# Kernel optimization log

Hardware: AMD Instinct MI355X
Metric: run time of the kernel (lower is better)

Reference implementation:

```python
import jax, jax.numpy as jnp
import numpy as np

DIM = 1024
HEADS = 16
HEAD_DIM = DIM // HEADS


def setup_inputs() -> dict:
    key = jax.random.key(0)
    ks = jax.random.split(key, 9)
    s = 1.0 / np.sqrt(DIM)
    return {
        "x": jax.random.normal(ks[0], (2, 2048, 1, DIM), dtype=jnp.float32),
        "Wq": jax.random.normal(ks[1], (DIM, DIM), dtype=jnp.float32) * s,
        "bq": jnp.zeros((DIM,), dtype=jnp.float32),
        "Wk": jax.random.normal(ks[2], (DIM, DIM), dtype=jnp.float32) * s,
        "bk": jnp.zeros((DIM,), dtype=jnp.float32),
        "Wv": jax.random.normal(ks[3], (DIM, DIM), dtype=jnp.float32) * s,
        "bv": jnp.zeros((DIM,), dtype=jnp.float32),
        "Wo": jax.random.normal(ks[4], (DIM, DIM), dtype=jnp.float32) * s,
        "bo": jnp.zeros((DIM,), dtype=jnp.float32),
    }


def reference(x, Wq, bq, Wk, bk, Wv, bv, Wo, bo):
    b, t, _, d = x.shape
    h, hd = HEADS, HEAD_DIM
    # torch Linear: y = x @ W.T + b
    q = (x @ Wq.T + bq).reshape(b, t, h, hd)
    k = (x @ Wk.T + bk).reshape(b, t, h, hd)
    v = (x @ Wv.T + bv).reshape(b, t, h, hd)
    # Source applies self.scaling (hd**-0.5) in torch AND divides by
    # sqrt(k_features) inside the jax chunk routine -> net scale 1/hd.
    q = q * (1.0 / hd)
    # key_chunk_size >= T -> one chunk; online softmax == exact stable softmax
    scores = jnp.einsum('bqhd,bkhd->bhqk', q, k)  # [B,H,T,T]
    w = jax.nn.softmax(scores, axis=-1)
    o = jnp.einsum('bhqk,bkhd->bqhd', w, v).reshape(b, t, d)
    return o @ Wo.T + bo
```

## Files before the change

kernel.cpp:

```cpp
#include <hip/hip_runtime.h>
#include <math.h>

typedef _Float16 f16;
typedef _Float16 f16x2 __attribute__((ext_vector_type(2)));
typedef _Float16 f16x4 __attribute__((ext_vector_type(4)));
typedef _Float16 f16x8 __attribute__((ext_vector_type(8)));
typedef float    f32x4 __attribute__((ext_vector_type(4)));

constexpr int DIM   = 1024;
constexpr int HEADS = 16;
constexpr int HD    = 64;
constexpr int BATCH = 2;
constexpr int SEQ   = 2048;
constexpr int MTOT  = BATCH * SEQ;
constexpr int NT2   = SEQ / 128;

#define QSCALE (1.4426950408889634f / 64.0f)

#define MFMA16(a, b, c) __builtin_amdgcn_mfma_f32_16x16x32_f16((a), (b), (c), 0, 0, 0)

__device__ __forceinline__ void glds16(const void* g, void* l) {
    __builtin_amdgcn_global_load_lds(
        (const __attribute__((address_space(1))) void*)g,
        (__attribute__((address_space(3))) void*)l, 16, 0, 0);
}

__device__ __forceinline__ float exp2_hw(float x) {
    float r;
    asm("v_exp_f32 %0, %1" : "=v"(r) : "v"(x));
    return r;
}

__device__ __forceinline__ f16x2 pk_f16(float a, float b) {
    return __builtin_bit_cast(f16x2, __builtin_amdgcn_cvt_pkrtz(a, b));
}

__global__ __launch_bounds__(256) void presplit_kernel(
    const float* __restrict__ x,  const float* __restrict__ Wq,
    const float* __restrict__ Wk, const float* __restrict__ Wv,
    const float* __restrict__ Wo,
    f16* __restrict__ Xh,  f16* __restrict__ WqH, f16* __restrict__ WkH,
    f16* __restrict__ WvH, f16* __restrict__ WoH)
{
    const int bid = blockIdx.x;
    const float* src; f16* dh; int row;
    if (bid < 4096)      { src = x;  dh = Xh;  row = bid; }
    else if (bid < 5120) { src = Wq; dh = WqH; row = bid - 4096; }
    else if (bid < 6144) { src = Wk; dh = WkH; row = bid - 5120; }
    else if (bid < 7168) { src = Wv; dh = WvH; row = bid - 6144; }
    else                 { src = Wo; dh = WoH; row = bid - 7168; }

    const int k = threadIdx.x * 4;
    const float4 v = *reinterpret_cast<const float4*>(&src[(size_t)row * DIM + k]);
    const int s = (row >> 1) & 3;
    const size_t o = (size_t)row * DIM + (k & ~31) + ((k & 31) ^ (s << 3));
    f16x4 h4;
    h4[0] = (f16)v.x; h4[1] = (f16)v.y; h4[2] = (f16)v.z; h4[3] = (f16)v.w;
    *reinterpret_cast<f16x4*>(&dh[o]) = h4;
}

template <int MODE>
__device__ __forceinline__ void gemm_plane_body(
    const f16* __restrict__ AhG, const f16* __restrict__ BhG,
    const float* __restrict__ bias, float* __restrict__ C,
    f16* __restrict__ F, float scale, f16* __restrict__ smem)
{
    const int tid = threadIdx.x;
    const int l   = tid & 63;
    const int w   = tid >> 6;
    const int wm  = (w >> 1) * 64;
    const int wn  = (w & 1) * 64;
    const int m0  = blockIdx.y * 128;
    const int n0  = blockIdx.x * 128;
    const int fr  = l & 15;
    const int fk  = (l >> 4) * 8;
    const int rg  = (l >> 4) * 4;
    const int fko = fk ^ (((fr >> 1) & 3) << 3);

    f32x4 acc[4][4] = {};

#define GSTAGE(B, K0) do {                                                  \
        _Pragma("unroll")                                                   \
        for (int j = 0; j < 4; ++j) {                                       \
            const int c = w * 4 + j;                             \
            const int p = c >> 3;                         \
            const f16* P = (p == 0) ? AhG : BhG;                            \
            const int r0 = (p == 0) ? m0 : n0;                              \
            const int row = r0 + (c & 7) * 16 + (l >> 2);                   \
            glds16(P + (size_t)row * DIM + (K0) + (l & 3) * 8,              \
                   smem + (B) * 8192 + c * 512);                            \
        }                                                                   \
    } while (0)

    GSTAGE(0, 0);
    GSTAGE(1, 32);
    int b0 = 0, b1 = 1, b2 = 2;

    for (int k0 = 0; k0 < DIM; k0 += 32) {
        if (k0 + 64 < DIM) {
            GSTAGE(b2, k0 + 64);
            asm volatile("s_waitcnt vmcnt(8)\ns_barrier" ::: "memory");
        } else if (k0 + 32 < DIM) {
            asm volatile("s_waitcnt vmcnt(4)\ns_barrier" ::: "memory");
        } else {
            asm volatile("s_waitcnt vmcnt(0)\ns_barrier" ::: "memory");
        }

        const f16* Ah = smem + b0 * 8192;
        const f16* Bh = Ah + 4096;

        f16x8 ah[4], bh[4];
        #pragma unroll
        for (int m = 0; m < 4; ++m)
            ah[m] = *reinterpret_cast<const f16x8*>(&Ah[(wm + m * 16 + fr) * 32 + fko]);
        #pragma unroll
        for (int n = 0; n < 4; ++n)
            bh[n] = *reinterpret_cast<const f16x8*>(&Bh[(wn + n * 16 + fr) * 32 + fko]);
        #pragma unroll
        for (int n = 0; n < 4; ++n)
            #pragma unroll
            for (int m = 0; m < 4; ++m) {
                if (MODE == 1)
                    acc[m][n] = MFMA16(bh[n], ah[m], acc[m][n]);
                else
                    acc[m][n] = MFMA16(ah[m], bh[n], acc[m][n]);
            }
        asm volatile("s_barrier" ::: "memory");
        const int tmp = b0; b0 = b1; b1 = b2; b2 = tmp;
    }
#undef GSTAGE

    if (MODE == 0 || MODE == 3) {
        #pragma unroll
        for (int n = 0; n < 4; ++n) {
            const int col  = n0 + wn + n * 16 + fr;
            const float bb = bias[col];
            #pragma unroll
            for (int m = 0; m < 4; ++m) {
                #pragma unroll
                for (int r = 0; r < 4; ++r) {
                    const int row = m0 + wm + m * 16 + rg + r;
                    const float v = (acc[m][n][r] + bb) * scale;
                    if (MODE == 0) C[(size_t)row * DIM + col] = v;
                    else           F[(size_t)row * DIM + col] = (f16)v;
                }
            }
        }
    } else if (MODE == 1) {
        constexpr int RS = 72;
        const int batch = m0 >> 11;
        const int kvg0  = m0 & 2047;
        for (int s = 0; s < 2; ++s) {
            __syncthreads();
            if ((w & 1) == s) {
                #pragma unroll
                for (int n = 0; n < 4; ++n) {
                    #pragma unroll
                    for (int m = 0; m < 4; ++m) {
                        const int kvrow = wm + m * 16 + fr;
                        const int dd    = n * 16 + rg;
                        f16x4 h4;
                        #pragma unroll
                        for (int r = 0; r < 4; ++r)
                            h4[r] = (f16)(acc[m][n][r] + bias[n0 + wn + dd + r]);
                        const int o = kvrow * RS + (dd ^ ((kvrow & 7) << 3));
                        *reinterpret_cast<f16x4*>(&smem[o]) = h4;
                    }
                }
            }
            __syncthreads();
            const size_t bh_ = (size_t)batch * HEADS + (n0 >> 6) + s;
            const int row = tid >> 1, c0 = (tid & 1) * 32;
            #pragma unroll
            for (int j = 0; j < 4; ++j) {
                const int so = row * RS + c0 + j * 8;
                const size_t go = bh_ * 131072 + (size_t)(kvg0 + row) * 64 + c0 + j * 8;
                *reinterpret_cast<f16x8*>(&F[go]) =
                    *reinterpret_cast<const f16x8*>(&smem[so]);
            }
        }
    } else {
        constexpr int RS = 136;
        const int batch = m0 >> 11;
        const int kvg0  = m0 & 2047;
        for (int s = 0; s < 2; ++s) {
            __syncthreads();
            if ((w & 1) == s) {
                #pragma unroll
                for (int n = 0; n < 4; ++n) {
                    const int d    = n * 16 + fr;
                    const float bb = bias[n0 + wn + d];
                    #pragma unroll
                    for (int m = 0; m < 4; ++m) {
                        const int kvl = wm + m * 16 + rg;
                        f16x4 h4;
                        h4[0] = (f16)(acc[m][n][0] + bb);
                        h4[1] = (f16)(acc[m][n][1] + bb);
                        h4[2] = (f16)(acc[m][n][2] + bb);
                        h4[3] = (f16)(acc[m][n][3] + bb);
                        const int o = d * RS + (kvl ^ ((d & 7) << 3));
                        *reinterpret_cast<f16x4*>(&smem[o]) = h4;
                    }
                }
            }
            __syncthreads();
            const size_t bh_ = (size_t)batch * HEADS + (n0 >> 6) + s;
            const int row = tid >> 2, c0 = (tid & 3) * 32;
            #pragma unroll
            for (int j = 0; j < 4; ++j) {
                const int so = row * RS + c0 + j * 8;
                const size_t go = bh_ * 131072 + (size_t)row * 2048 + kvg0 + c0 + j * 8;
                *reinterpret_cast<f16x8*>(&F[go]) =
                    *reinterpret_cast<const f16x8*>(&smem[so]);
            }
        }
    }
}

__global__ __launch_bounds__(256) void qkv_kernel(
    const f16* __restrict__ XhG,
    const f16* __restrict__ WqH, const float* __restrict__ bq,
    const f16* __restrict__ WkH, const float* __restrict__ bk,
    const f16* __restrict__ WvH, const float* __restrict__ bv,
    f16* __restrict__ QhG, f16* __restrict__ KhG, f16* __restrict__ VhG)
{
    __shared__ __align__(16) f16 smem[24576];
    if (blockIdx.z == 0)
        gemm_plane_body<3>(XhG, WqH, bq, nullptr, QhG, QSCALE, smem);
    else if (blockIdx.z == 1)
        gemm_plane_body<1>(XhG, WkH, bk, nullptr, KhG, 1.0f, smem);
    else
        gemm_plane_body<2>(XhG, WvH, bv, nullptr, VhG, 1.0f, smem);
}

__global__ __launch_bounds__(256) void oproj_kernel(
    const f16* __restrict__ OhG, const f16* __restrict__ WoH,
    const float* __restrict__ bo, float* __restrict__ out)
{
    __shared__ __align__(16) f16 smem[24576];
    gemm_plane_body<0>(OhG, WoH, bo, out, nullptr, 1.0f, smem);
}

__global__ __launch_bounds__(256, 2) void attn_kernel(
    const f16* __restrict__ QhG, const f16* __restrict__ KhG,
    const f16* __restrict__ VhG, f16* __restrict__ OhG)
{
    __shared__ __align__(16) f16 lds[2][2][8192];
    __shared__ __align__(16) f16 PL[4][2][1024];

    const int tid = threadIdx.x;
    const int l   = tid & 63;
    const int w   = tid >> 6;
    const int fr  = l & 15;
    const int g   = l >> 4;
    const int fk  = g * 8;
    const int rg  = g * 4;
    const int swz = (fr & 7) << 3;

    const int lin  = blockIdx.x + 16 * (blockIdx.y + 16 * blockIdx.z);
    const int sid  = (lin & 7) * 64 + (lin >> 3);
    const int qblk = sid & 15;
    const int head = (sid >> 4) & 15;
    const int batch = sid >> 8;

    const int q0 = qblk * 128;
    const size_t rowbase = (size_t)batch * SEQ;
    const int hcol = head * HD;
    const size_t bhbase = ((size_t)batch * HEADS + head) * (size_t)(SEQ * HD);

    size_t kA[4], vA[4];
    #pragma unroll
    for (int c = 0; c < 4; ++c) {
        const int h0 = (w * 4 + c) * 512 + l * 8;
        kA[c] = bhbase + (size_t)h0;
        vA[c] = bhbase + (size_t)(h0 >> 7) * 2048 + (h0 & 127);
    }

#define STAGE(B, T) do {                                                    \
        const size_t _ko = (size_t)(T) * 8192;                              \
        const size_t _vo = (size_t)(T) * 128;                               \
        _Pragma("unroll")                                                   \
        for (int c = 0; c < 4; ++c) {                                       \
            const int lo_ = (w * 4 + c) * 512;                              \
            glds16(KhG + kA[c] + _ko, &lds[B][0][lo_]);                     \
            glds16(VhG + vA[c] + _vo, &lds[B][1][lo_]);                     \
        }                                                                   \
    } while (0)

    STAGE(0, 0);

    f16x8 qh[2][2];
    #pragma unroll
    for (int qb = 0; qb < 2; ++qb) {
        const f16* qp = &QhG[(rowbase + q0 + w * 32 + qb * 16 + fr) * DIM + hcol];
        qh[qb][0] = *reinterpret_cast<const f16x8*>(&qp[fk]);
        qh[qb][1] = *reinterpret_cast<const f16x8*>(&qp[32 + fk]);
    }

    f16x8 onesv;
    #pragma unroll
    for (int i = 0; i < 8; ++i) onesv[i] = (f16)1.0f;

    f32x4 ls[2] = {};
    f32x4 oa[4][2] = {};

    int cur = 0;
    for (int t = 0; t < NT2; ++t) {
        asm volatile("s_waitcnt vmcnt(0) lgkmcnt(0)\ns_barrier" ::: "memory");
        if (t + 1 < NT2) STAGE(cur ^ 1, t + 1);

        #pragma unroll
        for (int hh = 0; hh < 2; ++hh) {
            const f16* Kh = &lds[cur][0][hh * 4096];
            const f16* Vh = &lds[cur][1][hh * 64];

            f32x4 sa[4][2] = {};
            __builtin_amdgcn_s_setprio(1);
            #pragma unroll
            for (int kvb = 0; kvb < 4; ++kvb) {
                #pragma unroll
                for (int ks = 0; ks < 2; ++ks) {
                    const int o = ((kvb * 16 + fr) * 64 + ks * 32 + fk) ^ swz;
                    const f16x8 kh = *reinterpret_cast<const f16x8*>(&Kh[o]);
                    sa[kvb][0] = MFMA16(kh, qh[0][ks], sa[kvb][0]);
                    sa[kvb][1] = MFMA16(kh, qh[1][ks], sa[kvb][1]);
                }
            }
            __builtin_amdgcn_s_setprio(0);

            f16x8 pf[2][2];
            #pragma unroll
            for (int qb = 0; qb < 2; ++qb) {
                f16* Wh = &PL[w][qb][0];
                #pragma unroll
                for (int kvb = 0; kvb < 4; ++kvb) {
                    const f16x2 p01 = pk_f16(exp2_hw(sa[kvb][qb][0]),
                                             exp2_hw(sa[kvb][qb][1]));
                    const f16x2 p23 = pk_f16(exp2_hw(sa[kvb][qb][2]),
                                             exp2_hw(sa[kvb][qb][3]));
                    f16x4 h4;
                    h4[0] = p01[0]; h4[1] = p01[1]; h4[2] = p23[0]; h4[3] = p23[1];
                    const int po = (fr * 64 + kvb * 16 + rg) ^ swz;
                    *reinterpret_cast<f16x4*>(&Wh[po]) = h4;
                }
                #pragma unroll
                for (int ks = 0; ks < 2; ++ks) {
                    const int ro = (fr * 64 + ks * 32 + fk) ^ swz;
                    pf[qb][ks] = *reinterpret_cast<const f16x8*>(&Wh[ro]);
                }
            }

            __builtin_amdgcn_s_setprio(1);
            #pragma unroll
            for (int qb = 0; qb < 2; ++qb)
                #pragma unroll
                for (int ks = 0; ks < 2; ++ks)
                    ls[qb] = MFMA16(onesv, pf[qb][ks], ls[qb]);
            #pragma unroll
            for (int db = 0; db < 4; ++db) {
                #pragma unroll
                for (int ks = 0; ks < 2; ++ks) {
                    const int vo = (db * 16 + fr) * 128 + ((ks * 32 + fk) ^ swz);
                    const f16x8 vh = *reinterpret_cast<const f16x8*>(&Vh[vo]);
                    oa[db][0] = MFMA16(vh, pf[0][ks], oa[db][0]);
                    oa[db][1] = MFMA16(vh, pf[1][ks], oa[db][1]);
                }
            }
            __builtin_amdgcn_s_setprio(0);
        }
        cur ^= 1;
    }
#undef STAGE

    #pragma unroll
    for (int qb = 0; qb < 2; ++qb) {
        const float inv = 1.0f / ls[qb][0];
        const size_t row = rowbase + q0 + w * 32 + qb * 16 + fr;
        const int s = ((int)row >> 1) & 3;
        #pragma unroll
        for (int db = 0; db < 4; ++db) {
            f16x4 h4;
            #pragma unroll
            for (int j = 0; j < 4; ++j) h4[j] = (f16)(oa[db][qb][j] * inv);
            const int kg = hcol + db * 16 + rg;
            const size_t o = row * DIM + (kg & ~31) + ((kg & 31) ^ (s << 3));
            *reinterpret_cast<f16x4*>(&OhG[o]) = h4;
        }
    }
}

extern "C" void kernel_launch(void* const* d_in, const int* in_sizes, int n_in,
                              void* d_out, int out_size, void* d_ws, size_t ws_size,
                              hipStream_t stream)
{
    const float* x  = (const float*)d_in[0];
    const float* Wq = (const float*)d_in[1];
    const float* bq = (const float*)d_in[2];
    const float* Wk = (const float*)d_in[3];
    const float* bk = (const float*)d_in[4];
    const float* Wv = (const float*)d_in[5];
    const float* bv = (const float*)d_in[6];
    const float* Wo = (const float*)d_in[7];
    const float* bo = (const float*)d_in[8];
    float* out = (float*)d_out;

    const size_t PS = (size_t)MTOT * DIM;
    f16* QhG = (f16*)d_ws;
    f16* KhG = QhG + PS;
    f16* VhG = KhG + PS;
    f16* XhG = VhG + PS;
    f16* WqH = XhG + PS;
    f16* WkH = WqH + (size_t)DIM * DIM;
    f16* WvH = WkH + (size_t)DIM * DIM;
    f16* WoH = WvH + (size_t)DIM * DIM;
    f16* OhG = XhG;

    presplit_kernel<<<8192, 256, 0, stream>>>(x, Wq, Wk, Wv, Wo,
                                              XhG, WqH, WkH, WvH, WoH);

    dim3 gqkv(DIM / 128, MTOT / 128, 3);
    qkv_kernel<<<gqkv, 256, 0, stream>>>(XhG, WqH, bq, WkH, bk, WvH, bv,
                                         QhG, KhG, VhG);

    dim3 gattn(SEQ / 128, HEADS, BATCH);
    attn_kernel<<<gattn, 256, 0, stream>>>(QhG, KhG, VhG, OhG);

    dim3 gout(DIM / 128, MTOT / 128);
    oproj_kernel<<<gout, 256, 0, stream>>>(OhG, WoH, bo, out);
}
```

Before: 112.4 us.

## Fuse Q, K, V projections into one block sharing the X tile

The QKV projection now runs one block per output tile that computes Q, K and V together. Each of the four waves stages one operand (X, Wq, Wk or Wv), so the X tile is loaded from global memory once instead of three times. The block keeps three accumulator sets and uses 96KB of shared memory with launch bounds of one block per CU. That cuts the grid to a third and lowers occupancy, and with fewer blocks per CU the load latency may be harder to hide. The attention kernel's V staging addresses and LDS offsets are also rewritten to a 64-wide row stride.

Result: no change. 110.9 us (-1.4%).

```diff
diff --git a/kernel.cpp b/kernel.cpp
--- a/kernel.cpp
+++ b/kernel.cpp
@@ -59,12 +59,15 @@
     *reinterpret_cast<f16x4*>(&dh[o]) = h4;
 }
 
-template <int MODE>
-__device__ __forceinline__ void gemm_plane_body(
-    const f16* __restrict__ AhG, const f16* __restrict__ BhG,
-    const float* __restrict__ bias, float* __restrict__ C,
-    f16* __restrict__ F, float scale, f16* __restrict__ smem)
-{
+__global__ __launch_bounds__(256, 1) void qkv_kernel(
+    const f16* __restrict__ XhG,
+    const f16* __restrict__ WqH, const float* __restrict__ bq,
+    const f16* __restrict__ WkH, const float* __restrict__ bk,
+    const f16* __restrict__ WvH, const float* __restrict__ bv,
+    f16* __restrict__ QhG, f16* __restrict__ KhG, f16* __restrict__ VhG)
+{
+    __shared__ __align__(16) f16 smem[49152];
+
     const int tid = threadIdx.x;
     const int l   = tid & 63;
     const int w   = tid >> 6;
@@ -77,13 +80,168 @@
     const int rg  = (l >> 4) * 4;
     const int fko = fk ^ (((fr >> 1) & 3) << 3);
 
+    const f16* Pw = (w == 0) ? XhG : (w == 1) ? WqH : (w == 2) ? WkH : WvH;
+    const int  r0w = (w == 0) ? m0 : n0;
+
+    f32x4 accq[4][4] = {}, acck[4][4] = {}, accv[4][4] = {};
+
+#define GSTAGE(B, K0) do {                                                  \
+        _Pragma("unroll")                                                   \
+        for (int j = 0; j < 8; ++j) {                                       \
+            const int row = r0w + j * 16 + (l >> 2);                        \
+            glds16(Pw + (size_t)row * DIM + (K0) + (l & 3) * 8,             \
+                   smem + (B) * 16384 + w * 4096 + j * 512);                \
+        }                                                                   \
+    } while (0)
+
+    GSTAGE(0, 0);
+    GSTAGE(1, 32);
+    int b0 = 0, b1 = 1, b2 = 2;
+
+    for (int k0 = 0; k0 < DIM; k0 += 32) {
+        if (k0 + 64 < DIM) {
+            GSTAGE(b2, k0 + 64);
+            asm volatile("s_waitcnt vmcnt(16)\ns_barrier" ::: "memory");
+        } else if (k0 + 32 < DIM) {
+            asm volatile("s_waitcnt vmcnt(8)\ns_barrier" ::: "memory");
+        } else {
+            asm volatile("s_waitcnt vmcnt(0)\ns_barrier" ::: "memory");
+        }
+
+        const f16* Bu = smem + b0 * 16384;
+        f16x8 ah[4], bqf[4], bkf[4], bvf[4];
+        #pragma unroll
+        for (int m = 0; m < 4; ++m)
+            ah[m] = *reinterpret_cast<const f16x8*>(&Bu[(wm + m * 16 + fr) * 32 + fko]);
+        #pragma unroll
+        for (int n = 0; n < 4; ++n) {
+            const int r = (wn + n * 16 + fr) * 32 + fko;
+            bqf[n] = *reinterpret_cast<const f16x8*>(&Bu[4096 + r]);
+            bkf[n] = *reinterpret_cast<const f16x8*>(&Bu[8192 + r]);
+            bvf[n] = *reinterpret_cast<const f16x8*>(&Bu[12288 + r]);
+        }
+        #pragma unroll
+        for (int n = 0; n < 4; ++n)
+            #pragma unroll
+            for (int m = 0; m < 4; ++m) {
+                accq[m][n] = MFMA16(ah[m], bqf[n], accq[m][n]);
+                acck[m][n] = MFMA16(bkf[n], ah[m], acck[m][n]);
+                accv[m][n] = MFMA16(ah[m], bvf[n], accv[m][n]);
+            }
+        asm volatile("s_barrier" ::: "memory");
+        const int tmp = b0; b0 = b1; b1 = b2; b2 = tmp;
+    }
+#undef GSTAGE
+
+    #pragma unroll
+    for (int n = 0; n < 4; ++n) {
+        const int col  = n0 + wn + n * 16 + fr;
+        const float bb = bq[col];
+        #pragma unroll
+        for (int m = 0; m < 4; ++m)
+            #pragma unroll
+            for (int r = 0; r < 4; ++r) {
+                const int row = m0 + wm + m * 16 + rg + r;
+                QhG[(size_t)row * DIM + col] = (f16)((accq[m][n][r] + bb) * QSCALE);
+            }
+    }
+
+    const int batch = m0 >> 11;
+    const int kvg0  = m0 & 2047;
+
+    {
+        constexpr int RS = 72;
+        for (int s = 0; s < 2; ++s) {
+            __syncthreads();
+            if ((w & 1) == s) {
+                #pragma unroll
+                for (int n = 0; n < 4; ++n) {
+                    #pragma unroll
+                    for (int m = 0; m < 4; ++m) {
+                        const int kvrow = wm + m * 16 + fr;
+                        const int dd    = n * 16 + rg;
+                        f16x4 h4;
+                        #pragma unroll
+                        for (int r = 0; r < 4; ++r)
+                            h4[r] = (f16)(acck[m][n][r] + bk[n0 + wn + dd + r]);
+                        const int o = kvrow * RS + (dd ^ ((kvrow & 7) << 3));
+                        *reinterpret_cast<f16x4*>(&smem[o]) = h4;
+                    }
+                }
+            }
+            __syncthreads();
+            const size_t bh_ = (size_t)batch * HEADS + (n0 >> 6) + s;
+            const int row = tid >> 1, c0 = (tid & 1) * 32;
+            #pragma unroll
+            for (int j = 0; j < 4; ++j) {
+                const int so = row * RS + c0 + j * 8;
+                const size_t go = bh_ * 131072 + (size_t)(kvg0 + row) * 64 + c0 + j * 8;
+                *reinterpret_cast<f16x8*>(&KhG[go]) =
+                    *reinterpret_cast<const f16x8*>(&smem[so]);
+            }
+        }
+    }
+
+    {
+        constexpr int RS = 136;
+        for (int s = 0; s < 2; ++s) {
+            __syncthreads();
+            if ((w & 1) == s) {
+                #pragma unroll
+                for (int n = 0; n < 4; ++n) {
+                    const int d    = n * 16 + fr;
+                    const float bb = bv[n0 + wn + d];
+                    #pragma unroll
+                    for (int m = 0; m < 4; ++m) {
+                        const int kvl = wm + m * 16 + rg;
+                        f16x4 h4;
+                        h4[0] = (f16)(accv[m][n][0] + bb);
+                        h4[1] = (f16)(accv[m][n][1] + bb);
+                        h4[2] = (f16)(accv[m][n][2] + bb);
+                        h4[3] = (f16)(accv[m][n][3] + bb);
+                        const int o = d * RS + (kvl ^ ((d & 7) << 3));
+                        *reinterpret_cast<f16x4*>(&smem[o]) = h4;
+                    }
+                }
+            }
+            __syncthreads();
+            const size_t bh_ = (size_t)batch * HEADS + (n0 >> 6) + s;
+            const int row = tid >> 2, c0 = (tid & 3) * 32;
+            #pragma unroll
+            for (int j = 0; j < 4; ++j) {
+                const int so = row * RS + c0 + j * 8;
+                const size_t go = bh_ * 131072 + (size_t)row * 2048 + kvg0 + c0 + j * 8;
+                *reinterpret_cast<f16x8*>(&VhG[go]) =
+                    *reinterpret_cast<const f16x8*>(&smem[so]);
+            }
+        }
+    }
+}
+
+__device__ __forceinline__ void gemm_oproj_body(
+    const f16* __restrict__ AhG, const f16* __restrict__ BhG,
+    const float* __restrict__ bias, float* __restrict__ C,
+    f16* __restrict__ smem)
+{
+    const int tid = threadIdx.x;
+    const int l   = tid & 63;
+    const int w   = tid >> 6;
+    const int wm  = (w >> 1) * 64;
+    const int wn  = (w & 1) * 64;
+    const int m0  = blockIdx.y * 128;
+    const int n0  = blockIdx.x * 128;
+    const int fr  = l & 15;
+    const int fk  = (l >> 4) * 8;
+    const int rg  = (l >> 4) * 4;
+    const int fko = fk ^ (((fr >> 1) & 3) << 3);
+
     f32x4 acc[4][4] = {};
 
 #define GSTAGE(B, K0) do {                                                  \
         _Pragma("unroll")                                                   \
         for (int j = 0; j < 4; ++j) {                                       \
-            const int c = w * 4 + j;                             \
-            const int p = c >> 3;                         \
+            const int c = w * 4 + j;                                        \
+            const int p = c >> 3;                                           \
             const f16* P = (p == 0) ? AhG : BhG;                            \
             const int r0 = (p == 0) ? m0 : n0;                              \
             const int row = r0 + (c & 7) * 16 + (l >> 2);                   \
@@ -119,118 +277,25 @@
         #pragma unroll
         for (int n = 0; n < 4; ++n)
             #pragma unroll
-            for (int m = 0; m < 4; ++m) {
-                if (MODE == 1)
-                    acc[m][n] = MFMA16(bh[n], ah[m], acc[m][n]);
-                else
-                    acc[m][n] = MFMA16(ah[m], bh[n], acc[m][n]);
-            }
+            for (int m = 0; m < 4; ++m)
+                acc[m][n] = MFMA16(ah[m], bh[n], acc[m][n]);
         asm volatile("s_barrier" ::: "memory");
         const int tmp = b0; b0 = b1; b1 = b2; b2 = tmp;
     }
 #undef GSTAGE
 
-    if (MODE == 0 || MODE == 3) {
-        #pragma unroll
-        for (int n = 0; n < 4; ++n) {
-            const int col  = n0 + wn + n * 16 + fr;
-            const float bb = bias[col];
-            #pragma unroll
-            for (int m = 0; m < 4; ++m) {
-                #pragma unroll
-                for (int r = 0; r < 4; ++r) {
-                    const int row = m0 + wm + m * 16 + rg + r;
-                    const float v = (acc[m][n][r] + bb) * scale;
-                    if (MODE == 0) C[(size_t)row * DIM + col] = v;
-                    else           F[(size_t)row * DIM + col] = (f16)v;
-                }
-            }
-        }
-    } else if (MODE == 1) {
-        constexpr int RS = 72;
-        const int batch = m0 >> 11;
-        const int kvg0  = m0 & 2047;
-        for (int s = 0; s < 2; ++s) {
-            __syncthreads();
-            if ((w & 1) == s) {
-                #pragma unroll
-                for (int n = 0; n < 4; ++n) {
-                    #pragma unroll
-                    for (int m = 0; m < 4; ++m) {
-                        const int kvrow = wm + m * 16 + fr;
-                        const int dd    = n * 16 + rg;
-                        f16x4 h4;
-                        #pragma unroll
-                        for (int r = 0; r < 4; ++r)
-                            h4[r] = (f16)(acc[m][n][r] + bias[n0 + wn + dd + r]);
-                        const int o = kvrow * RS + (dd ^ ((kvrow & 7) << 3));
-                        *reinterpret_cast<f16x4*>(&smem[o]) = h4;
-                    }
-                }
-            }
-            __syncthreads();
-            const size_t bh_ = (size_t)batch * HEADS + (n0 >> 6) + s;
-            const int row = tid >> 1, c0 = (tid & 1) * 32;
-            #pragma unroll
-            for (int j = 0; j < 4; ++j) {
-                const int so = row * RS + c0 + j * 8;
-                const size_t go = bh_ * 131072 + (size_t)(kvg0 + row) * 64 + c0 + j * 8;
-                *reinterpret_cast<f16x8*>(&F[go]) =
-                    *reinterpret_cast<const f16x8*>(&smem[so]);
-            }
-        }
-    } else {
-        constexpr int RS = 136;
-        const int batch = m0 >> 11;
-        const int kvg0  = m0 & 2047;
-        for (int s = 0; s < 2; ++s) {
-            __syncthreads();
-            if ((w & 1) == s) {
-                #pragma unroll
-                for (int n = 0; n < 4; ++n) {
-                    const int d    = n * 16 + fr;
-                    const float bb = bias[n0 + wn + d];
-                    #pragma unroll
-                    for (int m = 0; m < 4; ++m) {
-                        const int kvl = wm + m * 16 + rg;
-                        f16x4 h4;
-                        h4[0] = (f16)(acc[m][n][0] + bb);
-                        h4[1] = (f16)(acc[m][n][1] + bb);
-                        h4[2] = (f16)(acc[m][n][2] + bb);
-                        h4[3] = (f16)(acc[m][n][3] + bb);
-                        const int o = d * RS + (kvl ^ ((d & 7) << 3));
-                        *reinterpret_cast<f16x4*>(&smem[o]) = h4;
-                    }
-                }
-            }
-            __syncthreads();
-            const size_t bh_ = (size_t)batch * HEADS + (n0 >> 6) + s;
-            const int row = tid >> 2, c0 = (tid & 3) * 32;
-            #pragma unroll
-            for (int j = 0; j < 4; ++j) {
-                const int so = row * RS + c0 + j * 8;
-                const size_t go = bh_ * 131072 + (size_t)row * 2048 + kvg0 + c0 + j * 8;
-                *reinterpret_cast<f16x8*>(&F[go]) =
-                    *reinterpret_cast<const f16x8*>(&smem[so]);
-            }
-        }
-    }
-}
-
-__global__ __launch_bounds__(256) void qkv_kernel(
-    const f16* __restrict__ XhG,
-    const f16* __restrict__ WqH, const float* __restrict__ bq,
-    const f16* __restrict__ WkH, const float* __restrict__ bk,
-    const f16* __restrict__ WvH, const float* __restrict__ bv,
-    f16* __restrict__ QhG, f16* __restrict__ KhG, f16* __restrict__ VhG)
-{
-    __shared__ __align__(16) f16 smem[24576];
-    if (blockIdx.z == 0)
-        gemm_plane_body<3>(XhG, WqH, bq, nullptr, QhG, QSCALE, smem);
-    else if (blockIdx.z == 1)
-        gemm_plane_body<1>(XhG, WkH, bk, nullptr, KhG, 1.0f, smem);
-    else
-        gemm_plane_body<2>(XhG, WvH, bv, nullptr, VhG, 1.0f, smem);
+    #pragma unroll
+    for (int n = 0; n < 4; ++n) {
+        const int col  = n0 + wn + n * 16 + fr;
+        const float bb = bias[col];
+        #pragma unroll
+        for (int m = 0; m < 4; ++m)
+            #pragma unroll
+            for (int r = 0; r < 4; ++r) {
+                const int row = m0 + wm + m * 16 + rg + r;
+                C[(size_t)row * DIM + col] = acc[m][n][r] + bb;
+            }
+    }
 }
 
 __global__ __launch_bounds__(256) void oproj_kernel(
@@ -238,7 +303,7 @@
     const float* __restrict__ bo, float* __restrict__ out)
 {
     __shared__ __align__(16) f16 smem[24576];
-    gemm_plane_body<0>(OhG, WoH, bo, out, nullptr, 1.0f, smem);
+    gemm_oproj_body(OhG, WoH, bo, out, smem);
 }
 
 __global__ __launch_bounds__(256, 2) void attn_kernel(
@@ -273,7 +338,8 @@
     for (int c = 0; c < 4; ++c) {
         const int h0 = (w * 4 + c) * 512 + l * 8;
         kA[c] = bhbase + (size_t)h0;
-        vA[c] = bhbase + (size_t)(h0 >> 7) * 2048 + (h0 & 127);
+        vA[c] = bhbase + (size_t)((h0 >> 6) & 63) * 2048
+              + (size_t)(h0 >> 12) * 64 + (h0 & 63);
     }
 
 #define STAGE(B, T) do {                                                    \
@@ -312,7 +378,7 @@
         #pragma unroll
         for (int hh = 0; hh < 2; ++hh) {
             const f16* Kh = &lds[cur][0][hh * 4096];
-            const f16* Vh = &lds[cur][1][hh * 64];
+            const f16* Vh = &lds[cur][1][hh * 4096];
 
             f32x4 sa[4][2] = {};
             __builtin_amdgcn_s_setprio(1);
@@ -360,7 +426,7 @@
             for (int db = 0; db < 4; ++db) {
                 #pragma unroll
                 for (int ks = 0; ks < 2; ++ks) {
-                    const int vo = (db * 16 + fr) * 128 + ((ks * 32 + fk) ^ swz);
+                    const int vo = (db * 16 + fr) * 64 + ((ks * 32 + fk) ^ swz);
                     const f16x8 vh = *reinterpret_cast<const f16x8*>(&Vh[vo]);
                     oa[db][0] = MFMA16(vh, pf[0][ks], oa[db][0]);
                     oa[db][1] = MFMA16(vh, pf[1][ks], oa[db][1]);
@@ -418,7 +484,7 @@
     presplit_kernel<<<8192, 256, 0, stream>>>(x, Wq, Wk, Wv, Wo,
                                               XhG, WqH, WkH, WvH, WoH);
 
-    dim3 gqkv(DIM / 128, MTOT / 128, 3);
+    dim3 gqkv(DIM / 128, MTOT / 128);
     qkv_kernel<<<gqkv, 256, 0, stream>>>(XhG, WqH, bq, WkH, bk, WvH, bv,
                                          QhG, KhG, VhG);
 
```
